# Optimization experiments

Hardware: AMD Instinct MI355X
Metric: run time of the kernel (lower is better)

Reference implementation:

```python
import jax, jax.numpy as jnp
import numpy as np

N = 100000
E = 1600000
BN_EPS = 1e-5
# (in_channels, heads, out_channels, concat) per GATv2 layer
LAYERS = [(22, 3, 18, True), (54, 3, 14, True), (42, 3, 12, True), (36, 5, 10, False)]


def setup_inputs() -> dict:
    key = jax.random.key(0)
    ks = iter(jax.random.split(key, 64))
    nrm = lambda shape, s=0.1: jax.random.normal(next(ks), shape, jnp.float32) * s
    d = {}
    d["x"] = jax.random.normal(next(ks), (N, 22), jnp.float32)
    d["edge_index"] = jax.random.randint(next(ks), (2, E), 0, N)
    for i, (cin, h, c, concat) in enumerate(LAYERS, 1):
        d[f"Wl{i}"] = nrm((cin, h * c))
        d[f"Wr{i}"] = nrm((cin, h * c))
        d[f"bl{i}"] = jnp.zeros((h * c,), jnp.float32)
        d[f"br{i}"] = jnp.zeros((h * c,), jnp.float32)
        d[f"att{i}"] = nrm((h, c))
        outd = h * c if concat else c
        d[f"b{i}"] = jnp.zeros((outd,), jnp.float32)
        d[f"g{i}"] = jnp.ones((outd,), jnp.float32)
        d[f"be{i}"] = jnp.zeros((outd,), jnp.float32)
        d[f"rm{i}"] = nrm((outd,))
        d[f"rv{i}"] = jax.random.uniform(next(ks), (outd,), jnp.float32, 0.5, 1.5)
    d["Wmu"] = nrm((10, 10)); d["bmu"] = jnp.zeros((10,), jnp.float32)
    d["Wlv"] = nrm((10, 10)); d["blv"] = jnp.zeros((10,), jnp.float32)
    return d


def _gatv2(x, Wl, Wr, bl, br, att, b, src, dst, H, C, concat):
    n = x.shape[0]
    xl = (x @ Wl + bl).reshape(n, H, C)  # source transform (also the message)
    xr = (x @ Wr + br).reshape(n, H, C)  # target transform
    m = jax.nn.leaky_relu(xl[src] + xr[dst], 0.2)          # [Etot, H, C]
    e = jnp.einsum('ehc,hc->eh', m, att)                   # [Etot, H]
    emax = jax.lax.stop_gradient(jax.ops.segment_max(e, dst, num_segments=n))
    ex = jnp.exp(e - emax[dst])
    den = jax.ops.segment_sum(ex, dst, num_segments=n)     # [n, H]
    alpha = ex / den[dst]
    out = jax.ops.segment_sum(xl[src] * alpha[..., None], dst, num_segments=n)
    out = out.reshape(n, H * C) if concat else out.mean(axis=1)
    return out + b


def _bn(x, g, be, rm, rv):
    return g * (x - rm) * jax.lax.rsqrt(rv + BN_EPS) + be


def _fwd(p, edge_index):
    n = p["x"].shape[0]
    loop = jnp.arange(n)  # PyG GATv2Conv adds self-loops by default
    src = jnp.concatenate([edge_index[0], loop])
    dst = jnp.concatenate([edge_index[1], loop])
    h = p["x"]
    for i, (cin, H, C, concat) in enumerate(LAYERS, 1):
        h = _gatv2(h, p[f"Wl{i}"], p[f"Wr{i}"], p[f"bl{i}"], p[f"br{i}"],
                   p[f"att{i}"], p[f"b{i}"], src, dst, H, C, concat)
        h = _bn(h, p[f"g{i}"], p[f"be{i}"], p[f"rm{i}"], p[f"rv{i}"])
        if i == 1:  # source applies ELU only after bn1
            h = jax.nn.elu(h)
    mu = h @ p["Wmu"] + p["bmu"]
    log_var = h @ p["Wlv"] + p["blv"]
    return mu, log_var


def reference(x, edge_index, Wl1, Wr1, bl1, br1, att1, b1, g1, be1, rm1, rv1, Wl2, Wr2, bl2, br2, att2, b2, g2, be2, rm2, rv2, Wl3, Wr3, bl3, br3, att3, b3, g3, be3, rm3, rv3, Wl4, Wr4, bl4, br4, att4, b4, g4, be4, rm4, rv4, Wmu, bmu, Wlv, blv):
    p = {k: v for k, v in locals().items() if k != "edge_index"}
    return _fwd(p, edge_index)
```

## Files before the change

kernel.cpp:

```cpp
#include <hip/hip_runtime.h>

#define BN_EPS 1e-5f

typedef _Float16 half_t;
typedef _Float16 half2_t __attribute__((ext_vector_type(2)));

#define NBK_MAX 512
#define EPB 4096


__global__ void __launch_bounds__(256) bucket_count_kernel(
    const int* __restrict__ ei, int* __restrict__ bcnt, int E, int etot, int nbk) {
  __shared__ int lh[NBK_MAX];
  for (int i = threadIdx.x; i < nbk; i += 256) lh[i] = 0;
  __syncthreads();
  int base = blockIdx.x * EPB;
  int cnt = min(EPB, etot - base);
  for (int i = threadIdx.x; i < cnt; i += 256) {
    int e = base + i;
    int d = (e < E) ? ei[E + e] : (e - E);
    atomicAdd(&lh[d >> 8], 1);
  }
  __syncthreads();
  for (int i = threadIdx.x; i < nbk; i += 256)
    if (lh[i]) atomicAdd(&bcnt[i], lh[i]);
}

__global__ void __launch_bounds__(512) scan_buckets_kernel(
    const int* __restrict__ bcnt, int* __restrict__ boff, int* __restrict__ bcur,
    int nbk, int etot) {
  __shared__ int wsum[8];
  int tid = threadIdx.x, lane = tid & 63, wid = tid >> 6;
  int v = (tid < nbk) ? bcnt[tid] : 0;
  int incl = v;
#pragma unroll
  for (int off = 1; off < 64; off <<= 1) {
    int t = __shfl_up(incl, off, 64);
    if (lane >= off) incl += t;
  }
  if (lane == 63) wsum[wid] = incl;
  __syncthreads();
  if (wid == 0 && lane < 8) {
    int s = wsum[lane];
#pragma unroll
    for (int off = 1; off < 8; off <<= 1) {
      int t = __shfl_up(s, off, 8);
      if (lane >= off) s += t;
    }
    wsum[lane] = s;
  }
  __syncthreads();
  int woff = (wid > 0) ? wsum[wid - 1] : 0;
  int ex = incl + woff - v;
  if (tid < nbk) { boff[tid] = ex; bcur[tid] = ex; }
  if (tid == 0) boff[nbk] = etot;
}

__global__ void __launch_bounds__(256) bucket_scatter_kernel(
    const int* __restrict__ ei, int* __restrict__ bcur, int2* __restrict__ bstage,
    int E, int etot, int nbk) {
  __shared__ int2 se[EPB];
  __shared__ int lh[NBK_MAX], lbase[NBK_MAX];
  int base = blockIdx.x * EPB;
  int cnt = min(EPB, etot - base);
  for (int i = threadIdx.x; i < nbk; i += 256) lh[i] = 0;
  __syncthreads();
  for (int i = threadIdx.x; i < cnt; i += 256) {
    int e = base + i;
    int s, d;
    if (e < E) { s = ei[e]; d = ei[E + e]; } else { s = e - E; d = s; }
    se[i] = make_int2(s, d);
    atomicAdd(&lh[d >> 8], 1);
  }
  __syncthreads();
  for (int i = threadIdx.x; i < nbk; i += 256) {
    int c = lh[i];
    lbase[i] = c ? atomicAdd(&bcur[i], c) : 0;
    lh[i] = 0;
  }
  __syncthreads();
  for (int i = threadIdx.x; i < cnt; i += 256) {
    int2 sd = se[i];
    int b = sd.y >> 8;
    int r = atomicAdd(&lh[b], 1);
    bstage[lbase[b] + r] = sd;
  }
}

__global__ void __launch_bounds__(256) deg_count_kernel(
    const int2* __restrict__ bstage, const int* __restrict__ boff,
    int* __restrict__ deg, int n) {
  __shared__ int ld[256];
  int b = blockIdx.x;
  int d0 = b << 8;
  ld[threadIdx.x] = 0;
  __syncthreads();
  int p0 = boff[b], p1 = boff[b + 1];
  for (int p = p0 + threadIdx.x; p < p1; p += 256)
    atomicAdd(&ld[bstage[p].y - d0], 1);
  __syncthreads();
  int i = d0 + threadIdx.x;
  if (i < n) deg[i] = ld[threadIdx.x];
}

__global__ void __launch_bounds__(256) block_sum_kernel(const int* __restrict__ deg,
                                                        int* __restrict__ bsum, int n) {
  __shared__ int ws[4];
  int base = blockIdx.x * 1024;
  int s = 0;
  for (int i = threadIdx.x; i < 1024; i += 256) {
    int idx = base + i;
    s += (idx < n) ? deg[idx] : 0;
  }
#pragma unroll
  for (int off = 32; off; off >>= 1) s += __shfl_down(s, off, 64);
  int lane = threadIdx.x & 63, wid = threadIdx.x >> 6;
  if (lane == 0) ws[wid] = s;
  __syncthreads();
  if (threadIdx.x == 0) bsum[blockIdx.x] = ws[0] + ws[1] + ws[2] + ws[3];
}

__global__ void __launch_bounds__(1024) scan_sums_kernel(int* __restrict__ bsum, int nb) {
  __shared__ int wsum[16];
  int tid = threadIdx.x, lane = tid & 63, wid = tid >> 6;
  int v = (tid < nb) ? bsum[tid] : 0;
  int incl = v;
#pragma unroll
  for (int off = 1; off < 64; off <<= 1) {
    int t = __shfl_up(incl, off, 64);
    if (lane >= off) incl += t;
  }
  if (lane == 63) wsum[wid] = incl;
  __syncthreads();
  if (wid == 0 && lane < 16) {
    int s = wsum[lane];
#pragma unroll
    for (int off = 1; off < 16; off <<= 1) {
      int t = __shfl_up(s, off, 16);
      if (lane >= off) s += t;
    }
    wsum[lane] = s;
  }
  __syncthreads();
  int woff = (wid > 0) ? wsum[wid - 1] : 0;
  if (tid < nb) bsum[tid] = incl + woff - v;
}

__global__ void __launch_bounds__(1024) scan_block_kernel(const int* __restrict__ deg,
                                                          const int* __restrict__ boff,
                                                          int* __restrict__ indptr, int n) {
  __shared__ int wsum[16];
  int tid = threadIdx.x, lane = tid & 63, wid = tid >> 6;
  int i = blockIdx.x * 1024 + tid;
  int v = (i < n) ? deg[i] : 0;
  int incl = v;
#pragma unroll
  for (int off = 1; off < 64; off <<= 1) {
    int t = __shfl_up(incl, off, 64);
    if (lane >= off) incl += t;
  }
  if (lane == 63) wsum[wid] = incl;
  __syncthreads();
  if (wid == 0 && lane < 16) {
    int s = wsum[lane];
#pragma unroll
    for (int off = 1; off < 16; off <<= 1) {
      int t = __shfl_up(s, off, 16);
      if (lane >= off) s += t;
    }
    wsum[lane] = s;
  }
  __syncthreads();
  int woff = (wid > 0) ? wsum[wid - 1] : 0;
  if (i < n) indptr[i + 1] = incl + woff + boff[blockIdx.x];
  if (i == 0) indptr[0] = 0;
}

__global__ void __launch_bounds__(256) fine_place_kernel(
    const int2* __restrict__ bstage, const int* __restrict__ boff,
    const int* __restrict__ indptr, int* __restrict__ csrc, int n) {
  __shared__ int cur[256];
  int b = blockIdx.x;
  int d0 = b << 8;
  int i = d0 + threadIdx.x;
  cur[threadIdx.x] = (i < n) ? indptr[i] : 0;
  __syncthreads();
  int p0 = boff[b], p1 = boff[b + 1];
  for (int p = p0 + threadIdx.x; p < p1; p += 256) {
    int2 sd = bstage[p];
    int pos = atomicAdd(&cur[sd.y - d0], 1);
    csrc[pos] = sd.x;
  }
}


template <int CIN, int H, int C, int CPAD, int JT>
__global__ void __launch_bounds__(256) transform_kernel(
    const float* __restrict__ x, const float* __restrict__ Wl, const float* __restrict__ Wr,
    const float* __restrict__ bl, const float* __restrict__ br, half_t* __restrict__ xl,
    float* __restrict__ xr, int n) {
  constexpr int HC = H * C;
  constexpr int TPN = HC / JT;
  __shared__ float sW[2 * CIN * HC];
  for (int i = threadIdx.x; i < CIN * HC; i += blockDim.x) {
    sW[i] = Wl[i];
    sW[CIN * HC + i] = Wr[i];
  }
  __syncthreads();
  int idx = blockIdx.x * blockDim.x + threadIdx.x;
  if (idx >= n * TPN) return;
  int node = idx / TPN;
  int j0 = (idx - node * TPN) * JT;

  float al[JT], ar[JT];
#pragma unroll
  for (int jj = 0; jj < JT; jj++) {
    al[jj] = bl[j0 + jj];
    ar[jj] = br[j0 + jj];
  }
  const float2* xrow = reinterpret_cast<const float2*>(x + (size_t)node * CIN);
#pragma unroll
  for (int k2 = 0; k2 < CIN / 2; k2++) {
    float2 xv = xrow[k2];
#pragma unroll
    for (int q = 0; q < 2; q++) {
      float xs = q ? xv.y : xv.x;
      int k = 2 * k2 + q;
#pragma unroll
      for (int jj = 0; jj < JT; jj++) {
        al[jj] = fmaf(xs, sW[k * HC + j0 + jj], al[jj]);
        ar[jj] = fmaf(xs, sW[CIN * HC + k * HC + j0 + jj], ar[jj]);
      }
    }
  }
#pragma unroll
  for (int jj = 0; jj < JT; jj++) {
    int j = j0 + jj;
    int h = j / C, c = j - h * C;
    xl[((size_t)node * H + h) * CPAD + c] = (half_t)al[jj];
    xr[(size_t)node * HC + j] = ar[jj];
  }
}


#define IDX(K) csrc[p0 + (((K) < cnt) ? (K) : cnt - 1)]

#define ROW(B, IR)                                                                \
  {                                                                               \
    const uint4* xp_ = reinterpret_cast<const uint4*>(xlh + (size_t)(IR) * HCP);  \
    _Pragma("unroll") for (int i_ = 0; i_ < NB; i_++) B[i_] = xp_[i_];            \
  }

#define COMP_ROW(B, M)                                                                      \
  {                                                                                         \
    const half2_t* hp_ = reinterpret_cast<const half2_t*>(B);                               \
    float xs_[C];                                                                           \
    _Pragma("unroll") for (int i = 0; i < C / 2; i++) {                                     \
      xs_[2 * i] = (float)hp_[i].x;                                                         \
      xs_[2 * i + 1] = (float)hp_[i].y;                                                     \
    }                                                                                       \
    float e_ = 0.f;                                                                         \
    _Pragma("unroll") for (int c = 0; c < C; c++) {                                         \
      float m_ = xs_[c] + xr_reg[c];                                                        \
      m_ = (m_ > 0.f) ? m_ : 0.2f * m_;                                                     \
      e_ = fmaf(att_reg[c], m_, e_);                                                        \
    }                                                                                       \
    float ex_ = ((M) < cnt) ? __expf(e_) : 0.f;                                             \
    den += ex_;                                                                             \
    _Pragma("unroll") for (int c = 0; c < C; c++) acc[c] = fmaf(ex_, xs_[c], acc[c]);       \
  }

template <int H, int C, int CPAD, int MODE>
__global__ void __launch_bounds__(256) edge_kernel(
    const half_t* __restrict__ xl, const float* __restrict__ xr,
    const int* __restrict__ indptr, const int* __restrict__ csrc,
    const float* __restrict__ att, const float* __restrict__ bias,
    const float* __restrict__ g, const float* __restrict__ be,
    const float* __restrict__ rm, const float* __restrict__ rv,
    float* __restrict__ out, int n) {
  constexpr int HC = H * C;
  constexpr int HCP = H * CPAD;
  constexpr int NB = CPAD / 8;
  int t = blockIdx.x * blockDim.x + threadIdx.x;
  if (t >= n * H) return;
  int node = t / H;
  int h = t - node * H;

  float xr_reg[C], att_reg[C];
  const float2* xrp = reinterpret_cast<const float2*>(xr + (size_t)node * HC + h * C);
#pragma unroll
  for (int i = 0; i < C / 2; i++) {
    float2 v = xrp[i];
    xr_reg[2 * i] = v.x;
    xr_reg[2 * i + 1] = v.y;
  }
#pragma unroll
  for (int c = 0; c < C; c++) att_reg[c] = att[h * C + c];

  float acc[C];
#pragma unroll
  for (int c = 0; c < C; c++) acc[c] = 0.f;
  float den = 0.f;

  int p0 = indptr[node], p1 = indptr[node + 1];
  int cnt = p1 - p0;
  const half_t* xlh = xl + h * CPAD;

  uint4 B0[NB], B1[NB], B2[NB];
  int i0, i1, i2;
  i0 = IDX(0); i1 = IDX(1); i2 = IDX(2);
  ROW(B0, i0) ROW(B1, i1) ROW(B2, i2)
  i0 = IDX(3); i1 = IDX(4); i2 = IDX(5);
  int cnt3 = ((cnt + 2) / 3) * 3;
  for (int m = 0; m < cnt3; m += 3) {
    COMP_ROW(B0, m)     ROW(B0, i0) i0 = IDX(m + 6);
    COMP_ROW(B1, m + 1) ROW(B1, i1) i1 = IDX(m + 7);
    COMP_ROW(B2, m + 2) ROW(B2, i2) i2 = IDX(m + 8);
  }

  float inv = 1.f / den;
  float2* orow = reinterpret_cast<float2*>(out + (size_t)node * HC + h * C);
#pragma unroll
  for (int c2 = 0; c2 < C / 2; c2++) {
    float2 ov;
#pragma unroll
    for (int q = 0; q < 2; q++) {
      int c = 2 * c2 + q;
      float val = acc[c] * inv;
      if constexpr (MODE != 2) {
        int j = h * C + c;
        val += bias[j];
        float sc = g[j] * rsqrtf(rv[j] + BN_EPS);
        val = fmaf(sc, val - rm[j], be[j]);
        if constexpr (MODE == 1) val = (val > 0.f) ? val : expm1f(val);
      }
      if (q) ov.y = val; else ov.x = val;
    }
    orow[c2] = ov;
  }
}


__global__ void final_kernel(const float* __restrict__ r4, const float* __restrict__ b4,
                             const float* __restrict__ g4, const float* __restrict__ be4,
                             const float* __restrict__ rm4, const float* __restrict__ rv4,
                             const float* __restrict__ Wmu, const float* __restrict__ bmu,
                             const float* __restrict__ Wlv, const float* __restrict__ blv,
                             float* __restrict__ out, int n) {
  int node = blockIdx.x * blockDim.x + threadIdx.x;
  if (node >= n) return;
  float hsum[10];
#pragma unroll
  for (int c = 0; c < 10; c++) hsum[c] = 0.f;
  const float* r = r4 + (size_t)node * 50;
#pragma unroll
  for (int h = 0; h < 5; h++)
#pragma unroll
    for (int c = 0; c < 10; c++) hsum[c] += r[h * 10 + c];
  float hv[10];
#pragma unroll
  for (int c = 0; c < 10; c++) {
    float v = hsum[c] * 0.2f + b4[c];
    float sc = g4[c] * rsqrtf(rv4[c] + BN_EPS);
    hv[c] = fmaf(sc, v - rm4[c], be4[c]);
  }
#pragma unroll
  for (int j = 0; j < 10; j++) {
    float mu = bmu[j], lv = blv[j];
#pragma unroll
    for (int c = 0; c < 10; c++) {
      mu = fmaf(hv[c], Wmu[c * 10 + j], mu);
      lv = fmaf(hv[c], Wlv[c * 10 + j], lv);
    }
    out[(size_t)node * 10 + j] = mu;
    out[(size_t)n * 10 + (size_t)node * 10 + j] = lv;
  }
}


extern "C" void kernel_launch(void* const* d_in, const int* in_sizes, int n_in,
                              void* d_out, int out_size, void* d_ws, size_t ws_size,
                              hipStream_t stream) {
  const float* x = (const float*)d_in[0];
  const int* ei = (const int*)d_in[1];
  const int n = in_sizes[0] / 22;
  const int E = in_sizes[1] / 2;
  const int etot = E + n;
  const int nbk = (n + 255) >> 8;

  auto P = [&](int i) { return (const float*)d_in[i]; };

  char* ws = (char*)d_ws;
  size_t off = 0;
  auto alloc = [&](size_t bytes) -> void* {
    void* p = ws + off;
    off += (bytes + 255) & ~(size_t)255;
    return p;
  };
  half_t* xl = (half_t*)alloc((size_t)n * 80 * 2);
  float* xr = (float*)alloc((size_t)n * 54 * 4);
  float* hb = (float*)alloc((size_t)n * 54 * 4);
  int* deg = (int*)alloc((size_t)n * 4);
  int* indptr = (int*)alloc((size_t)(n + 1) * 4);
  int* csrc = (int*)alloc((size_t)etot * 4);
  int* bcnt = (int*)alloc((size_t)(nbk + 1) * 4);
  int* boff = (int*)alloc((size_t)(nbk + 1) * 4);
  int* bcur = (int*)alloc((size_t)(nbk + 1) * 4);
  int nb = (n + 1023) / 1024;
  int* bsum = (int*)alloc((size_t)nb * 4);
  int2* bstage = (int2*)xl;

  unsigned bb = (unsigned)((etot + EPB - 1) / EPB);
  unsigned nblk = (unsigned)((n + 255) / 256);

  hipMemsetAsync(bcnt, 0, (size_t)(nbk + 1) * 4, stream);
  bucket_count_kernel<<<bb, 256, 0, stream>>>(ei, bcnt, E, etot, nbk);
  scan_buckets_kernel<<<1, 512, 0, stream>>>(bcnt, boff, bcur, nbk, etot);
  bucket_scatter_kernel<<<bb, 256, 0, stream>>>(ei, bcur, bstage, E, etot, nbk);
  deg_count_kernel<<<(unsigned)nbk, 256, 0, stream>>>(bstage, boff, deg, n);
  block_sum_kernel<<<(unsigned)nb, 256, 0, stream>>>(deg, bsum, n);
  scan_sums_kernel<<<1, 1024, 0, stream>>>(bsum, nb);
  scan_block_kernel<<<(unsigned)nb, 1024, 0, stream>>>(deg, bsum, indptr, n);
  fine_place_kernel<<<(unsigned)nbk, 256, 0, stream>>>(bstage, boff, indptr, csrc, n);

  transform_kernel<22, 3, 18, 24, 6><<<(unsigned)(((size_t)n * 9 + 255) / 256), 256, 0, stream>>>(
      x, P(2), P(3), P(4), P(5), xl, xr, n);
  edge_kernel<3, 18, 24, 1><<<(unsigned)(((size_t)n * 3 + 255) / 256), 256, 0, stream>>>(
      xl, xr, indptr, csrc, P(6), P(7), P(8), P(9), P(10), P(11), hb, n);

  transform_kernel<54, 3, 14, 16, 6><<<(unsigned)(((size_t)n * 7 + 255) / 256), 256, 0, stream>>>(
      hb, P(12), P(13), P(14), P(15), xl, xr, n);
  edge_kernel<3, 14, 16, 0><<<(unsigned)(((size_t)n * 3 + 255) / 256), 256, 0, stream>>>(
      xl, xr, indptr, csrc, P(16), P(17), P(18), P(19), P(20), P(21), hb, n);

  transform_kernel<42, 3, 12, 16, 6><<<(unsigned)(((size_t)n * 6 + 255) / 256), 256, 0, stream>>>(
      hb, P(22), P(23), P(24), P(25), xl, xr, n);
  edge_kernel<3, 12, 16, 0><<<(unsigned)(((size_t)n * 3 + 255) / 256), 256, 0, stream>>>(
      xl, xr, indptr, csrc, P(26), P(27), P(28), P(29), P(30), P(31), hb, n);

  transform_kernel<36, 5, 10, 16, 10><<<(unsigned)(((size_t)n * 5 + 255) / 256), 256, 0, stream>>>(
      hb, P(32), P(33), P(34), P(35), xl, xr, n);
  edge_kernel<5, 10, 16, 2><<<(unsigned)(((size_t)n * 5 + 255) / 256), 256, 0, stream>>>(
      xl, xr, indptr, csrc, P(36), nullptr, nullptr, nullptr, nullptr, nullptr, hb, n);

  final_kernel<<<nblk, 256, 0, stream>>>(
      hb, P(37), P(38), P(39), P(40), P(41), P(42), P(43), P(44), P(45), (float*)d_out, n);
}
```

Measured before the change: 578.6 us.

## Sort nodes by degree for edge kernels and fuse degree-scan into bucket pass

```diff
diff --git a/kernel.cpp b/kernel.cpp
--- a/kernel.cpp
+++ b/kernel.cpp
@@ -87,43 +87,28 @@
   }
 }
 
-__global__ void __launch_bounds__(256) deg_count_kernel(
+__global__ void __launch_bounds__(256) deg_indptr_kernel(
     const int2* __restrict__ bstage, const int* __restrict__ boff,
-    int* __restrict__ deg, int n) {
+    int* __restrict__ deg, int* __restrict__ indptr, int* __restrict__ dhist, int n) {
   __shared__ int ld[256];
-  int b = blockIdx.x;
+  __shared__ int lh[64];
+  __shared__ int wsum[4];
+  int b = blockIdx.x, tid = threadIdx.x;
   int d0 = b << 8;
-  ld[threadIdx.x] = 0;
+  ld[tid] = 0;
+  if (tid < 64) lh[tid] = 0;
   __syncthreads();
   int p0 = boff[b], p1 = boff[b + 1];
-  for (int p = p0 + threadIdx.x; p < p1; p += 256)
+  for (int p = p0 + tid; p < p1; p += 256)
     atomicAdd(&ld[bstage[p].y - d0], 1);
   __syncthreads();
-  int i = d0 + threadIdx.x;
-  if (i < n) deg[i] = ld[threadIdx.x];
-}
-
-__global__ void __launch_bounds__(256) block_sum_kernel(const int* __restrict__ deg,
-                                                        int* __restrict__ bsum, int n) {
-  __shared__ int ws[4];
-  int base = blockIdx.x * 1024;
-  int s = 0;
-  for (int i = threadIdx.x; i < 1024; i += 256) {
-    int idx = base + i;
-    s += (idx < n) ? deg[idx] : 0;
-  }
-#pragma unroll
-  for (int off = 32; off; off >>= 1) s += __shfl_down(s, off, 64);
-  int lane = threadIdx.x & 63, wid = threadIdx.x >> 6;
-  if (lane == 0) ws[wid] = s;
-  __syncthreads();
-  if (threadIdx.x == 0) bsum[blockIdx.x] = ws[0] + ws[1] + ws[2] + ws[3];
-}
-
-__global__ void __launch_bounds__(1024) scan_sums_kernel(int* __restrict__ bsum, int nb) {
-  __shared__ int wsum[16];
-  int tid = threadIdx.x, lane = tid & 63, wid = tid >> 6;
-  int v = (tid < nb) ? bsum[tid] : 0;
+  int i = d0 + tid;
+  int v = ld[tid];
+  if (i < n) {
+    deg[i] = v;
+    atomicAdd(&lh[63 - min(v, 63)], 1);
+  }
+  int lane = tid & 63, wid = tid >> 6;
   int incl = v;
 #pragma unroll
   for (int off = 1; off < 64; off <<= 1) {
@@ -132,48 +117,49 @@
   }
   if (lane == 63) wsum[wid] = incl;
   __syncthreads();
-  if (wid == 0 && lane < 16) {
-    int s = wsum[lane];
-#pragma unroll
-    for (int off = 1; off < 16; off <<= 1) {
-      int t = __shfl_up(s, off, 16);
-      if (lane >= off) s += t;
-    }
-    wsum[lane] = s;
-  }
-  __syncthreads();
-  int woff = (wid > 0) ? wsum[wid - 1] : 0;
-  if (tid < nb) bsum[tid] = incl + woff - v;
-}
-
-__global__ void __launch_bounds__(1024) scan_block_kernel(const int* __restrict__ deg,
-                                                          const int* __restrict__ boff,
-                                                          int* __restrict__ indptr, int n) {
-  __shared__ int wsum[16];
-  int tid = threadIdx.x, lane = tid & 63, wid = tid >> 6;
-  int i = blockIdx.x * 1024 + tid;
-  int v = (i < n) ? deg[i] : 0;
+  if (tid == 0) {
+    int s = 0;
+#pragma unroll
+    for (int w = 0; w < 4; w++) { int t = wsum[w]; wsum[w] = s; s += t; }
+  }
+  __syncthreads();
+  incl += wsum[wid];
+  if (i < n) indptr[i + 1] = p0 + incl;
+  if (b == 0 && tid == 0) indptr[0] = 0;
+  __syncthreads();
+  if (tid < 64 && lh[tid]) atomicAdd(&dhist[tid], lh[tid]);
+}
+
+__global__ void __launch_bounds__(64) scan64_kernel(const int* __restrict__ dhist,
+                                                    int* __restrict__ dcur) {
+  int lane = threadIdx.x;
+  int v = dhist[lane];
   int incl = v;
 #pragma unroll
   for (int off = 1; off < 64; off <<= 1) {
     int t = __shfl_up(incl, off, 64);
     if (lane >= off) incl += t;
   }
-  if (lane == 63) wsum[wid] = incl;
-  __syncthreads();
-  if (wid == 0 && lane < 16) {
-    int s = wsum[lane];
-#pragma unroll
-    for (int off = 1; off < 16; off <<= 1) {
-      int t = __shfl_up(s, off, 16);
-      if (lane >= off) s += t;
-    }
-    wsum[lane] = s;
-  }
-  __syncthreads();
-  int woff = (wid > 0) ? wsum[wid - 1] : 0;
-  if (i < n) indptr[i + 1] = incl + woff + boff[blockIdx.x];
-  if (i == 0) indptr[0] = 0;
+  dcur[lane] = incl - v;
+}
+
+__global__ void __launch_bounds__(256) perm_kernel(const int* __restrict__ deg,
+                                                   int* __restrict__ dcur,
+                                                   int* __restrict__ perm, int n) {
+  __shared__ int lh[64], lbase[64];
+  if (threadIdx.x < 64) lh[threadIdx.x] = 0;
+  __syncthreads();
+  int i = blockIdx.x * blockDim.x + threadIdx.x;
+  int bk = 0, lr = 0;
+  if (i < n) {
+    bk = 63 - min(deg[i], 63);
+    lr = atomicAdd(&lh[bk], 1);
+  }
+  __syncthreads();
+  if (threadIdx.x < 64 && lh[threadIdx.x])
+    lbase[threadIdx.x] = atomicAdd(&dcur[threadIdx.x], lh[threadIdx.x]);
+  __syncthreads();
+  if (i < n) perm[lbase[bk] + lr] = i;
 }
 
 __global__ void __launch_bounds__(256) fine_place_kernel(
@@ -274,17 +260,18 @@
 __global__ void __launch_bounds__(256) edge_kernel(
     const half_t* __restrict__ xl, const float* __restrict__ xr,
     const int* __restrict__ indptr, const int* __restrict__ csrc,
-    const float* __restrict__ att, const float* __restrict__ bias,
-    const float* __restrict__ g, const float* __restrict__ be,
-    const float* __restrict__ rm, const float* __restrict__ rv,
-    float* __restrict__ out, int n) {
+    const int* __restrict__ perm, const float* __restrict__ att,
+    const float* __restrict__ bias, const float* __restrict__ g,
+    const float* __restrict__ be, const float* __restrict__ rm,
+    const float* __restrict__ rv, float* __restrict__ out, int n) {
   constexpr int HC = H * C;
   constexpr int HCP = H * CPAD;
   constexpr int NB = CPAD / 8;
   int t = blockIdx.x * blockDim.x + threadIdx.x;
   if (t >= n * H) return;
-  int node = t / H;
-  int h = t - node * H;
+  int slot = t / H;
+  int h = t - slot * H;
+  int node = perm[slot];
 
   float xr_reg[C], att_reg[C];
   const float2* xrp = reinterpret_cast<const float2*>(xr + (size_t)node * HC + h * C);
@@ -403,45 +390,45 @@
   int* deg = (int*)alloc((size_t)n * 4);
   int* indptr = (int*)alloc((size_t)(n + 1) * 4);
   int* csrc = (int*)alloc((size_t)etot * 4);
-  int* bcnt = (int*)alloc((size_t)(nbk + 1) * 4);
+  int* perm = (int*)alloc((size_t)n * 4);
+  int* bcnt = (int*)alloc((size_t)(nbk + 129) * 4);
+  int* dhist = bcnt + nbk + 1;
+  int* dcur = dhist + 64;
   int* boff = (int*)alloc((size_t)(nbk + 1) * 4);
   int* bcur = (int*)alloc((size_t)(nbk + 1) * 4);
-  int nb = (n + 1023) / 1024;
-  int* bsum = (int*)alloc((size_t)nb * 4);
   int2* bstage = (int2*)xl;
 
   unsigned bb = (unsigned)((etot + EPB - 1) / EPB);
   unsigned nblk = (unsigned)((n + 255) / 256);
 
-  hipMemsetAsync(bcnt, 0, (size_t)(nbk + 1) * 4, stream);
+  hipMemsetAsync(bcnt, 0, (size_t)(nbk + 129) * 4, stream);
   bucket_count_kernel<<<bb, 256, 0, stream>>>(ei, bcnt, E, etot, nbk);
   scan_buckets_kernel<<<1, 512, 0, stream>>>(bcnt, boff, bcur, nbk, etot);
   bucket_scatter_kernel<<<bb, 256, 0, stream>>>(ei, bcur, bstage, E, etot, nbk);
-  deg_count_kernel<<<(unsigned)nbk, 256, 0, stream>>>(bstage, boff, deg, n);
-  block_sum_kernel<<<(unsigned)nb, 256, 0, stream>>>(deg, bsum, n);
-  scan_sums_kernel<<<1, 1024, 0, stream>>>(bsum, nb);
-  scan_block_kernel<<<(unsigned)nb, 1024, 0, stream>>>(deg, bsum, indptr, n);
+  deg_indptr_kernel<<<(unsigned)nbk, 256, 0, stream>>>(bstage, boff, deg, indptr, dhist, n);
+  scan64_kernel<<<1, 64, 0, stream>>>(dhist, dcur);
+  perm_kernel<<<nblk, 256, 0, stream>>>(deg, dcur, perm, n);
   fine_place_kernel<<<(unsigned)nbk, 256, 0, stream>>>(bstage, boff, indptr, csrc, n);
 
   transform_kernel<22, 3, 18, 24, 6><<<(unsigned)(((size_t)n * 9 + 255) / 256), 256, 0, stream>>>(
       x, P(2), P(3), P(4), P(5), xl, xr, n);
   edge_kernel<3, 18, 24, 1><<<(unsigned)(((size_t)n * 3 + 255) / 256), 256, 0, stream>>>(
-      xl, xr, indptr, csrc, P(6), P(7), P(8), P(9), P(10), P(11), hb, n);
+      xl, xr, indptr, csrc, perm, P(6), P(7), P(8), P(9), P(10), P(11), hb, n);
 
   transform_kernel<54, 3, 14, 16, 6><<<(unsigned)(((size_t)n * 7 + 255) / 256), 256, 0, stream>>>(
       hb, P(12), P(13), P(14), P(15), xl, xr, n);
   edge_kernel<3, 14, 16, 0><<<(unsigned)(((size_t)n * 3 + 255) / 256), 256, 0, stream>>>(
-      xl, xr, indptr, csrc, P(16), P(17), P(18), P(19), P(20), P(21), hb, n);
+      xl, xr, indptr, csrc, perm, P(16), P(17), P(18), P(19), P(20), P(21), hb, n);
 
   transform_kernel<42, 3, 12, 16, 6><<<(unsigned)(((size_t)n * 6 + 255) / 256), 256, 0, stream>>>(
       hb, P(22), P(23), P(24), P(25), xl, xr, n);
   edge_kernel<3, 12, 16, 0><<<(unsigned)(((size_t)n * 3 + 255) / 256), 256, 0, stream>>>(
-      xl, xr, indptr, csrc, P(26), P(27), P(28), P(29), P(30), P(31), hb, n);
+      xl, xr, indptr, csrc, perm, P(26), P(27), P(28), P(29), P(30), P(31), hb, n);
 
   transform_kernel<36, 5, 10, 16, 10><<<(unsigned)(((size_t)n * 5 + 255) / 256), 256, 0, stream>>>(
       hb, P(32), P(33), P(34), P(35), xl, xr, n);
   edge_kernel<5, 10, 16, 2><<<(unsigned)(((size_t)n * 5 + 255) / 256), 256, 0, stream>>>(
-      xl, xr, indptr, csrc, P(36), nullptr, nullptr, nullptr, nullptr, nullptr, hb, n);
+      xl, xr, indptr, csrc, perm, P(36), nullptr, nullptr, nullptr, nullptr, nullptr, hb, n);
 
   final_kernel<<<nblk, 256, 0, stream>>>(
       hb, P(37), P(38), P(39), P(40), P(41), P(42), P(43), P(44), P(45), (float*)d_out, n);
```

Result: slower. 608.9 us (+5.2%).
